# Optimization experiments

Measured on AMD Instinct MI355X. Metric: run time of the kernel, lower is better.

The kernel has to match this reference:

```python
import jax, jax.numpy as jnp
import numpy as np

B, N, E, F, C = 4, 10000, 160000, 128, 128
NUM_ITERATIONS = 3  # num_iterations init arg


def setup_inputs() -> dict:
    key = jax.random.key(0)
    ks = jax.random.split(key, 8)
    objects = jax.random.normal(ks[0], (B, N, F), dtype=jnp.float32)
    connections = jax.random.randint(ks[1], (B, E, 2), 0, N, dtype=jnp.int32)
    # small init scales keep exp() in the attention numerically tame (mirrors
    # glorot/orthogonal-scale weights at init)
    object_state_W = jax.random.normal(ks[2], (F, C), dtype=jnp.float32) * (1.0 / np.sqrt(F))
    state_attention_W = jax.random.normal(ks[3], (C, C), dtype=jnp.float32) * 0.05
    linked_state_attention_W = jax.random.normal(ks[4], (C, C), dtype=jnp.float32) * 0.05
    linked_state_W = jax.random.normal(ks[5], (C, C), dtype=jnp.float32) * (1.0 / np.sqrt(C))
    attention_b = jnp.zeros((C,), dtype=jnp.float32)
    state_b = jnp.zeros((C,), dtype=jnp.float32)
    return {
        "objects": objects,
        "object_state_W": object_state_W,
        "state_attention_W": state_attention_W,
        "linked_state_attention_W": linked_state_attention_W,
        "attention_b": attention_b,
        "linked_state_W": linked_state_W,
        "state_b": state_b,
        "connections": connections,
    }


def reference(objects, object_state_W, state_attention_W, linked_state_attention_W,
              attention_b, linked_state_W, state_b, connections):
    # bidirectional: double edges with both orientations  [B, 2E]
    src = jnp.concatenate([connections[:, :, 0], connections[:, :, 1]], axis=1)
    dst = jnp.concatenate([connections[:, :, 1], connections[:, :, 0]], axis=1)

    # initial states: [B, N, C]
    states = jnp.tanh(jnp.einsum('bnf,fc->bnc', objects, object_state_W) + state_b)

    def step_one(states_b, src_b, dst_b):
        # states_b: [N, C]; src_b/dst_b: [2E]
        states_aW = states_b @ state_attention_W          # [N, C]
        linked_aW = states_b @ linked_state_attention_W   # [N, C]
        # per-edge unnormalized attention  [2E, C]
        attention = jnp.exp(states_aW[src_b] + linked_aW[dst_b] + attention_b)
        # scatter-add normalization; self edge contributes 1 (exp(0))
        attention_norm = jnp.ones_like(states_b).at[src_b].add(attention)  # [N, C]
        self_attention = 1.0 / attention_norm
        attention = attention / attention_norm[src_b]
        # weighted neighbor aggregation
        attented = attention * states_b[dst_b]                              # [2E, C]
        linked_gated = jnp.zeros_like(states_b).at[src_b].add(attented)     # [N, C]
        return jnp.tanh(states_b * self_attention + linked_gated @ linked_state_W + state_b)

    step = jax.vmap(step_one)
    for _ in range(NUM_ITERATIONS):
        states = step(states, src, dst)
    return states
```

## Files before the change

### kernel.cpp

```cpp
#include <hip/hip_runtime.h>
#include <hip/hip_bf16.h>


#define BATCH 4
#define NNODE 10000
#define NEDGE 160000
#define TWOE  (2*NEDGE)
#define MROWS (BATCH*NNODE)
#define NCHUNK 64
#define CHUNKE (NEDGE/NCHUNK)
#define PADN  10240

typedef unsigned short u16;
typedef unsigned int   u32;
typedef __attribute__((ext_vector_type(8))) short bf16x8_t;
typedef __attribute__((ext_vector_type(4))) float f32x4_t;

__device__ __forceinline__ float b2f(u16 h){ return __uint_as_float(((u32)h) << 16); }
__device__ __forceinline__ u16 f2bf(float f){
  u32 u = __float_as_uint(f);
  return (u16)((u + 0x7fffu + ((u >> 16) & 1u)) >> 16);
}
__device__ __forceinline__ float fast_tanh(float x){
  float e = __expf(2.0f * x);
  return fmaf(-2.0f, __builtin_amdgcn_rcpf(e + 1.0f), 1.0f);
}

__global__ void detect_dtype(const u32* __restrict__ objw, int* __restrict__ flag){
  __shared__ int zc, hc;
  if (threadIdx.x == 0){ zc = 0; hc = 0; }
  __syncthreads();
  int z = 0, h = 0;
  for (int i = threadIdx.x; i < 1024; i += 256){
    u32 lo = objw[i] & 0xffffu;
    if (lo == 0) z++;
    if (((lo >> 7) & 0xffu) >= 160u) h++;
  }
  atomicAdd(&zc, z); atomicAdd(&hc, h);
  __syncthreads();
  if (threadIdx.x == 0) *flag = (hc > 0 || zc > 512) ? 1 : 0;
}

__global__ void prep_weights(const void* __restrict__ Wo, const void* __restrict__ Wa,
                             const void* __restrict__ Wla, const void* __restrict__ Wl,
                             const void* __restrict__ ab, const void* __restrict__ sb,
                             const int* __restrict__ flag, u16* __restrict__ Wt,
                             float* __restrict__ biasf){
  int idx = blockIdx.x * 256 + threadIdx.x;
  bool f = (*flag != 0);
  if (idx < 65536){
    int m = idx >> 14, k = (idx >> 7) & 127, c = idx & 127;
    const void* src = (m == 0) ? Wo : (m == 1) ? Wa : (m == 2) ? Wla : Wl;
    u16 h = f ? f2bf(((const float*)src)[k * 128 + c]) : ((const u16*)src)[k * 128 + c];
    Wt[m * 16384 + c * 128 + k] = h;
  } else {
    int t = idx - 65536;
    const void* src = (t < 128) ? sb : ab;
    int i = t & 127;
    biasf[t] = f ? ((const float*)src)[i] : b2f(((const u16*)src)[i]);
  }
}

__device__ __forceinline__ void chunk_of(int blk, int& b, int& c){
  int xcd = blk & 7;
  b = xcd >> 1;
  c = ((blk >> 3) << 1) | (xcd & 1);
}

__global__ void __launch_bounds__(256) csr_hist(const int* __restrict__ conn,
                                                u16* __restrict__ partial){
  int b, c; chunk_of(blockIdx.x, b, c);
  __shared__ u32 hist[NNODE];
  for (int n = threadIdx.x; n < NNODE; n += 256) hist[n] = 0;
  __syncthreads();
  const int2* cp = (const int2*)conn + (size_t)b * NEDGE + c * CHUNKE;
  for (int i = threadIdx.x; i < CHUNKE; i += 256){
    int2 e = cp[i];
    atomicAdd(&hist[e.x], 1);
    atomicAdd(&hist[e.y], 1);
  }
  __syncthreads();
  u16* prow = partial + (size_t)(b * NCHUNK + c) * PADN;
  for (int n = threadIdx.x; n < NNODE; n += 256) prow[n] = (u16)hist[n];
}

__global__ void __launch_bounds__(256) csr_colscan(u16* __restrict__ partial,
    int* __restrict__ row_start, int* __restrict__ bsum){
  int b = blockIdx.x / 40, w = blockIdx.x % 40;
  int n = w * 256 + threadIdx.x;
  u32 run = 0;
  if (n < NNODE){
    #pragma unroll 8
    for (int c = 0; c < NCHUNK; c++){
      size_t idx = (size_t)(b * NCHUNK + c) * PADN + n;
      u32 v = partial[idx];
      partial[idx] = (u16)run;
      run += v;
    }
  }
  __shared__ u32 buf[256];
  buf[threadIdx.x] = run;
  __syncthreads();
  for (int off = 1; off < 256; off <<= 1){
    u32 x = (threadIdx.x >= (unsigned)off) ? buf[threadIdx.x - off] : 0;
    __syncthreads();
    buf[threadIdx.x] += x;
    __syncthreads();
  }
  u32 incl = buf[threadIdx.x];
  if (n < NNODE) row_start[b * (NNODE + 1) + n] = (int)(incl - run);
  if (threadIdx.x == 255) bsum[blockIdx.x] = (int)incl;
}

__global__ void scanB(const int* __restrict__ bsum, int* __restrict__ boff,
                      int* __restrict__ row_start){
  __shared__ int s[160];
  if (threadIdx.x < 160) s[threadIdx.x] = bsum[threadIdx.x];
  __syncthreads();
  if (threadIdx.x < 160){
    int b = threadIdx.x / 40, j = threadIdx.x % 40;
    int off = 0;
    for (int q = b * 40; q < b * 40 + j; q++) off += s[q];
    boff[threadIdx.x] = off;
  }
  if (threadIdx.x < BATCH) row_start[threadIdx.x * (NNODE + 1) + NNODE] = TWOE;
}

__global__ void scanC(int* __restrict__ row_start, const int* __restrict__ boff){
  int b = blockIdx.x / 40, j = blockIdx.x % 40;
  int n = j * 256 + threadIdx.x;
  if (n < NNODE) row_start[b * (NNODE + 1) + n] += boff[blockIdx.x];
}

__global__ void __launch_bounds__(256) csr_fill(const int* __restrict__ conn,
    const u16* __restrict__ partial, const int* __restrict__ row_start,
    int* __restrict__ edge_dst){
  int b, c; chunk_of(blockIdx.x, b, c);
  __shared__ u32 cur[NNODE];
  const u16* prow = partial + (size_t)(b * NCHUNK + c) * PADN;
  const int* rs = row_start + b * (NNODE + 1);
  for (int n = threadIdx.x; n < NNODE; n += 256) cur[n] = (u32)rs[n] + prow[n];
  __syncthreads();
  const int2* cp = (const int2*)conn + (size_t)b * NEDGE + c * CHUNKE;
  int* edb = edge_dst + (size_t)b * TWOE;
  for (int i = threadIdx.x; i < CHUNKE; i += 256){
    int2 e = cp[i];
    u32 p1 = atomicAdd(&cur[e.x], 1); edb[p1] = e.y;
    u32 p2 = atomicAdd(&cur[e.y], 1); edb[p2] = e.x;
  }
}

__device__ __forceinline__ void gemm_tile4(const u16* __restrict__ arow,
    const u16* __restrict__ wt, int lm, int lq, int cofs, f32x4_t acc[4]){
  #pragma unroll
  for (int ks = 0; ks < 4; ks++){
    bf16x8_t a = *(const bf16x8_t*)(arow + ks * 32);
    #pragma unroll
    for (int nb = 0; nb < 4; nb++){
      bf16x8_t bfr = *(const bf16x8_t*)(wt + (cofs + nb * 16 + lm) * 128 + ks * 32 + lq * 8);
      acc[nb] = __builtin_amdgcn_mfma_f32_16x16x32_bf16(a, bfr, acc[nb], 0, 0, 0);
    }
  }
}

__device__ __forceinline__ void gemm_tile4_packed(const u32* __restrict__ Lrow,
    const u16* __restrict__ wt, int lm, int lq, int cofs, f32x4_t acc[4]){
  #pragma unroll
  for (int ks = 0; ks < 4; ks++){
    uint4 wa = *(const uint4*)(Lrow + ks * 32 + lq * 8);
    uint4 wb = *(const uint4*)(Lrow + ks * 32 + lq * 8 + 4);
    bf16x8_t a;
    a[0] = (short)wa.x; a[1] = (short)wa.y; a[2] = (short)wa.z; a[3] = (short)wa.w;
    a[4] = (short)wb.x; a[5] = (short)wb.y; a[6] = (short)wb.z; a[7] = (short)wb.w;
    #pragma unroll
    for (int nb = 0; nb < 4; nb++){
      bf16x8_t bfr = *(const bf16x8_t*)(wt + (cofs + nb * 16 + lm) * 128 + ks * 32 + lq * 8);
      acc[nb] = __builtin_amdgcn_mfma_f32_16x16x32_bf16(a, bfr, acc[nb], 0, 0, 0);
    }
  }
}

__device__ __forceinline__ void phase2_awlaw4(const u16* __restrict__ ldstile,
    const u16* __restrict__ Wt, const float* __restrict__ biasf,
    int lm, int lq, int cofs, int r0, _Float16* __restrict__ eat,
    u32* __restrict__ ghw){
  const u16* Wta  = Wt + 16384;
  const u16* Wtla = Wt + 32768;
  const u16* ldsrow = ldstile + lm * 136 + lq * 8;
  f32x4_t accA[4], accL[4];
  #pragma unroll
  for (int i = 0; i < 4; i++){ accA[i] = (f32x4_t){0.f,0.f,0.f,0.f}; accL[i] = (f32x4_t){0.f,0.f,0.f,0.f}; }
  #pragma unroll
  for (int ks = 0; ks < 4; ks++){
    bf16x8_t a = *(const bf16x8_t*)(ldsrow + ks * 32);
    #pragma unroll
    for (int nb = 0; nb < 4; nb++){
      bf16x8_t ba = *(const bf16x8_t*)(Wta  + (cofs + nb * 16 + lm) * 128 + ks * 32 + lq * 8);
      bf16x8_t bl = *(const bf16x8_t*)(Wtla + (cofs + nb * 16 + lm) * 128 + ks * 32 + lq * 8);
      accA[nb] = __builtin_amdgcn_mfma_f32_16x16x32_bf16(a, ba, accA[nb], 0, 0, 0);
      accL[nb] = __builtin_amdgcn_mfma_f32_16x16x32_bf16(a, bl, accL[nb], 0, 0, 0);
    }
  }
  #pragma unroll
  for (int nb = 0; nb < 4; nb++){
    int col = cofs + nb * 16 + lm;
    float bb = biasf[128 + col];
    #pragma unroll
    for (int i = 0; i < 4; i++){
      int row = r0 + lq * 4 + i;
      float ea = fminf(__expf(accA[nb][i]), 60000.0f);
      eat[(lq * 4 + i) * 128 + col] = (_Float16)ea;
      _Float16 elh = (_Float16)fminf(__expf(accL[nb][i] + bb), 60000.0f);
      u16 sbf = ldstile[(lq * 4 + i) * 136 + col];
      _Float16 sh = (_Float16)b2f(sbf);
      u32 elu = (u32)(*(const u16*)&elh);
      u32 shu = (u32)(*(const u16*)&sh);
      ghw[(size_t)row * 64 + (col & 63)] = elu | (shu << 16);
    }
  }
}

__device__ __forceinline__ void eah_writeback(const _Float16* __restrict__ eat,
    _Float16* __restrict__ eah, int blk_r0, int tid){
  const uint4* src = (const uint4*)eat;
  uint4* dst = (uint4*)(eah + (size_t)blk_r0 * 128);
  dst[tid]       = src[tid];
  dst[tid + 256] = src[tid + 256];
}

__global__ void __launch_bounds__(256) fused_init(const void* __restrict__ obj_raw,
    const int* __restrict__ flag, const u16* __restrict__ Wt,
    const float* __restrict__ biasf, _Float16* __restrict__ eah,
    u32* __restrict__ gat0, u32* __restrict__ gat1){
  __shared__ u16 lds[2][16 * 136];
  __shared__ _Float16 eat[2][16 * 128];
  const int lane = threadIdx.x & 63, wave = threadIdx.x >> 6;
  const int t = wave >> 1, ch = wave & 1, cofs = ch * 64;
  const int r0 = blockIdx.x * 32 + t * 16;
  const int lm = lane & 15, lq = lane >> 4;
  f32x4_t acc[4];
  #pragma unroll
  for (int i = 0; i < 4; i++) acc[i] = (f32x4_t){0.f, 0.f, 0.f, 0.f};
  if (*flag){
    const float* arow = (const float*)obj_raw + (size_t)(r0 + lm) * 128 + lq * 8;
    #pragma unroll
    for (int ks = 0; ks < 4; ks++){
      float4 fa = *(const float4*)(arow + ks * 32);
      float4 fb = *(const float4*)(arow + ks * 32 + 4);
      bf16x8_t a;
      a[0] = (short)f2bf(fa.x); a[1] = (short)f2bf(fa.y);
      a[2] = (short)f2bf(fa.z); a[3] = (short)f2bf(fa.w);
      a[4] = (short)f2bf(fb.x); a[5] = (short)f2bf(fb.y);
      a[6] = (short)f2bf(fb.z); a[7] = (short)f2bf(fb.w);
      #pragma unroll
      for (int nb = 0; nb < 4; nb++){
        bf16x8_t bfr = *(const bf16x8_t*)(Wt + (cofs + nb * 16 + lm) * 128 + ks * 32 + lq * 8);
        acc[nb] = __builtin_amdgcn_mfma_f32_16x16x32_bf16(a, bfr, acc[nb], 0, 0, 0);
      }
    }
  } else {
    gemm_tile4((const u16*)obj_raw + (size_t)(r0 + lm) * 128 + lq * 8, Wt, lm, lq, cofs, acc);
  }
  #pragma unroll
  for (int nb = 0; nb < 4; nb++){
    int col = cofs + nb * 16 + lm;
    float bb = biasf[col];
    #pragma unroll
    for (int i = 0; i < 4; i++)
      lds[t][(lq * 4 + i) * 136 + col] = f2bf(fast_tanh(acc[nb][i] + bb));
  }
  __syncthreads();
  phase2_awlaw4(&lds[t][0], Wt, biasf, lm, lq, cofs, r0, &eat[t][0], ch ? gat1 : gat0);
  __syncthreads();
  eah_writeback(&eat[0][0], eah, blockIdx.x * 32, threadIdx.x);
}

__global__ void __launch_bounds__(256) fused_mid(const u32* __restrict__ lgsa,
    const u16* __restrict__ Wt, const float* __restrict__ biasf,
    _Float16* __restrict__ eah, u32* __restrict__ gat0, u32* __restrict__ gat1){
  __shared__ u16 lds[2][16 * 136];
  __shared__ _Float16 eat[2][16 * 128];
  const int lane = threadIdx.x & 63, wave = threadIdx.x >> 6;
  const int t = wave >> 1, ch = wave & 1, cofs = ch * 64;
  const int r0 = blockIdx.x * 32 + t * 16;
  const int lm = lane & 15, lq = lane >> 4;
  f32x4_t acc[4];
  #pragma unroll
  for (int i = 0; i < 4; i++) acc[i] = (f32x4_t){0.f, 0.f, 0.f, 0.f};
  gemm_tile4_packed(lgsa + (size_t)(r0 + lm) * 128, Wt + 49152, lm, lq, cofs, acc);
  #pragma unroll
  for (int nb = 0; nb < 4; nb++){
    int col = cofs + nb * 16 + lm;
    float bb = biasf[col];
    #pragma unroll
    for (int i = 0; i < 4; i++){
      int row = r0 + lq * 4 + i;
      u32 v = lgsa[(size_t)row * 128 + col];
      u16 hb = (u16)(v >> 16);
      float sa = (float)(*(const _Float16*)&hb);
      lds[t][(lq * 4 + i) * 136 + col] = f2bf(fast_tanh(sa + acc[nb][i] + bb));
    }
  }
  __syncthreads();
  phase2_awlaw4(&lds[t][0], Wt, biasf, lm, lq, cofs, r0, &eat[t][0], ch ? gat1 : gat0);
  __syncthreads();
  eah_writeback(&eat[0][0], eah, blockIdx.x * 32, threadIdx.x);
}

__global__ void __launch_bounds__(256) final_out(const u32* __restrict__ lgsa,
    const u16* __restrict__ Wt, const float* __restrict__ biasf,
    const int* __restrict__ flag, void* __restrict__ outp){
  const int lane = threadIdx.x & 63, wave = threadIdx.x >> 6;
  const int t = wave >> 1, ch = wave & 1, cofs = ch * 64;
  const int r0 = blockIdx.x * 32 + t * 16;
  const int lm = lane & 15, lq = lane >> 4;
  bool f32out = (*flag != 0);
  f32x4_t acc[4];
  #pragma unroll
  for (int i = 0; i < 4; i++) acc[i] = (f32x4_t){0.f, 0.f, 0.f, 0.f};
  gemm_tile4_packed(lgsa + (size_t)(r0 + lm) * 128, Wt + 49152, lm, lq, cofs, acc);
  #pragma unroll
  for (int nb = 0; nb < 4; nb++){
    int col = cofs + nb * 16 + lm;
    float bb = biasf[col];
    #pragma unroll
    for (int i = 0; i < 4; i++){
      int row = r0 + lq * 4 + i;
      u32 vv = lgsa[(size_t)row * 128 + col];
      u16 hb = (u16)(vv >> 16);
      float sa = (float)(*(const _Float16*)&hb);
      float v = fast_tanh(sa + acc[nb][i] + bb);
      if (f32out) ((float*)outp)[(size_t)row * 128 + col] = v;
      else        ((u16*)  outp)[(size_t)row * 128 + col] = f2bf(v);
    }
  }
}

__device__ __forceinline__ void acc_mix(u32 g, float one, float& a1, float& a2){
  asm("v_fma_mix_f32 %0, %2, %3, %0 op_sel:[0,0,0] op_sel_hi:[1,0,0]\n\t"
      "v_fma_mix_f32 %1, %2, %2, %1 op_sel:[0,1,0] op_sel_hi:[1,1,0]"
      : "+v"(a1), "+v"(a2)
      : "v"(g), "v"(one));
}

__global__ void __launch_bounds__(256) edge_kernel(const _Float16* __restrict__ eah,
    const u32* __restrict__ gat0, const u32* __restrict__ gat1,
    const int* __restrict__ row_start, const int* __restrict__ edge_dst,
    u32* __restrict__ lgsa){
  int blk = blockIdx.x;
  int xcd = blk & 7;
  int b = xcd >> 1, h = xcd & 1;
  int i = blk >> 3;
  int n = i * 4 + (int)(threadIdx.x >> 6);
  int node = b * NNODE + n;
  int c = threadIdx.x & 63;
  const u32* gh = (h ? gat1 : gat0) + (size_t)b * NNODE * 64;
  const u32* ghc = gh + c;
  int e0 = __builtin_amdgcn_readfirstlane(row_start[b * (NNODE + 1) + n]);
  int e1 = __builtin_amdgcn_readfirstlane(row_start[b * (NNODE + 1) + n + 1]);
  const int* ed = edge_dst + (size_t)b * TWOE;

  float ea = (float)eah[(size_t)node * 128 + h * 64 + c];
  u32 self = ghc[(size_t)n << 6];
  const float one = 1.0f;

  float s1 = 0.f, s2 = 0.f, t1 = 0.f, t2 = 0.f;
  int len = e1 - e0;
  int e = e0;
  int rem = len >> 3;
  int d[8];
  if (rem){
    #pragma unroll
    for (int j = 0; j < 8; j++) d[j] = ed[e0 + j];
  }
  for (; rem > 0; rem--){
    u32 g[8];
    #pragma unroll
    for (int j = 0; j < 8; j++) g[j] = ghc[(size_t)d[j] << 6];
    int ep = e + (rem > 1 ? 8 : 0);
    int dn[8];
    #pragma unroll
    for (int j = 0; j < 8; j++) dn[j] = ed[ep + j];
    #pragma unroll
    for (int j = 0; j < 8; j++) acc_mix(g[j], one, (j & 1) ? t1 : s1, (j & 1) ? t2 : s2);
    #pragma unroll
    for (int j = 0; j < 8; j++) d[j] = dn[j];
    e += 8;
  }
  for (; e < e1; e++){
    u32 gg = ghc[(size_t)ed[e] << 6];
    acc_mix(gg, one, s1, s2);
  }
  s1 += t1; s2 += t2;
  float inv = __builtin_amdgcn_rcpf(fmaf(ea, s1, 1.0f));
  float lg = ea * s2 * inv;
  u16 hb = (u16)(self >> 16);
  float s_self = (float)(*(const _Float16*)&hb);
  _Float16 hs = (_Float16)(s_self * inv);
  u32 pk = (u32)f2bf(lg) | ((u32)(*(const u16*)&hs) << 16);
  lgsa[(size_t)node * 128 + h * 64 + c] = pk;
}

extern "C" void kernel_launch(void* const* d_in, const int* in_sizes, int n_in,
                              void* d_out, int out_size, void* d_ws, size_t ws_size,
                              hipStream_t stream){
  (void)in_sizes; (void)n_in; (void)ws_size; (void)out_size;
  const void* objects = d_in[0];
  const void* Wo      = d_in[1];
  const void* Wa      = d_in[2];
  const void* Wla     = d_in[3];
  const void* attn_b  = d_in[4];
  const void* Wl      = d_in[5];
  const void* state_b = d_in[6];
  const int*  conn    = (const int*)d_in[7];

  char* base = (char*)d_ws;
  size_t off = 0;
  auto alloc = [&](size_t bytes) -> char* {
    char* p = base + off;
    off = (off + bytes + 255) & ~(size_t)255;
    return p;
  };
  int*      flag      = (int*)     alloc(256);
  u16*      Wt        = (u16*)     alloc((size_t)4 * 16384 * 2);
  float*    biasf     = (float*)   alloc(256 * 4);
  _Float16* eah       = (_Float16*)alloc((size_t)MROWS * 128 * 2);
  u32*      gat0      = (u32*)     alloc((size_t)MROWS * 64 * 4);
  u32*      gat1      = (u32*)     alloc((size_t)MROWS * 64 * 4);
  u32*      lgsa      = (u32*)     alloc((size_t)MROWS * 128 * 4);
  u16*      partial   = (u16*)     alloc((size_t)BATCH * NCHUNK * PADN * 2);
  int*      row_start = (int*)     alloc((size_t)BATCH * (NNODE + 1) * 4);
  int*      edge_dst  = (int*)     alloc((size_t)BATCH * TWOE * 4);
  int*      bsum      = (int*)     alloc(160 * 4);
  int*      boff      = (int*)     alloc(160 * 4);

  detect_dtype<<<1, 256, 0, stream>>>((const u32*)objects, flag);
  prep_weights<<<257, 256, 0, stream>>>(Wo, Wa, Wla, Wl, attn_b, state_b, flag, Wt, biasf);

  csr_hist<<<256, 256, 0, stream>>>(conn, partial);
  csr_colscan<<<160, 256, 0, stream>>>(partial, row_start, bsum);
  scanB<<<1, 256, 0, stream>>>(bsum, boff, row_start);
  scanC<<<160, 256, 0, stream>>>(row_start, boff);
  csr_fill<<<256, 256, 0, stream>>>(conn, partial, row_start, edge_dst);

  fused_init<<<MROWS / 32, 256, 0, stream>>>(objects, flag, Wt, biasf, eah, gat0, gat1);
  edge_kernel<<<MROWS / 2, 256, 0, stream>>>(eah, gat0, gat1, row_start, edge_dst, lgsa);
  fused_mid<<<MROWS / 32, 256, 0, stream>>>(lgsa, Wt, biasf, eah, gat0, gat1);
  edge_kernel<<<MROWS / 2, 256, 0, stream>>>(eah, gat0, gat1, row_start, edge_dst, lgsa);
  fused_mid<<<MROWS / 32, 256, 0, stream>>>(lgsa, Wt, biasf, eah, gat0, gat1);
  edge_kernel<<<MROWS / 2, 256, 0, stream>>>(eah, gat0, gat1, row_start, edge_dst, lgsa);
  final_out<<<MROWS / 32, 256, 0, stream>>>(lgsa, Wt, biasf, flag, d_out);
}
```

Baseline: 375.6 us.

## Pad CSR rows to multiples of eight with zero sentinel nodes for tail-free gather

Each node's adjacency list is padded to a multiple of 8 entries, and the padding points at per-batch sentinel rows whose gathered values are zeroed, so the edge kernel no longer needs a scalar tail loop. The edge kernel reads indices with readfirstlane as scalars, double-buffers two groups of 8 gathers ahead of the accumulation, and sets an occupancy launch bound. This costs two extra setup kernels, a degree buffer and a larger edge array. The main risk is that the sentinel indexing across batches must land exactly on the zeroed rows.

```diff
diff --git a/kernel.cpp b/kernel.cpp
--- a/kernel.cpp
+++ b/kernel.cpp
@@ -10,6 +10,7 @@
 #define NCHUNK 64
 #define CHUNKE (NEDGE/NCHUNK)
 #define PADN  10240
+#define EDPAD (TWOE + 8*NNODE)
 
 typedef unsigned short u16;
 typedef unsigned int   u32;
@@ -85,7 +86,7 @@
 }
 
 __global__ void __launch_bounds__(256) csr_colscan(u16* __restrict__ partial,
-    int* __restrict__ row_start, int* __restrict__ bsum){
+    int* __restrict__ row_start, int* __restrict__ bsum, int* __restrict__ deg){
   int b = blockIdx.x / 40, w = blockIdx.x % 40;
   int n = w * 256 + threadIdx.x;
   u32 run = 0;
@@ -98,8 +99,9 @@
       run += v;
     }
   }
+  u32 pad = (run + 7u) & ~7u;
   __shared__ u32 buf[256];
-  buf[threadIdx.x] = run;
+  buf[threadIdx.x] = pad;
   __syncthreads();
   for (int off = 1; off < 256; off <<= 1){
     u32 x = (threadIdx.x >= (unsigned)off) ? buf[threadIdx.x - off] : 0;
@@ -108,7 +110,10 @@
     __syncthreads();
   }
   u32 incl = buf[threadIdx.x];
-  if (n < NNODE) row_start[b * (NNODE + 1) + n] = (int)(incl - run);
+  if (n < NNODE){
+    row_start[b * (NNODE + 1) + n] = (int)(incl - pad);
+    deg[b * NNODE + n] = (int)run;
+  }
   if (threadIdx.x == 255) bsum[blockIdx.x] = (int)incl;
 }
 
@@ -123,7 +128,11 @@
     for (int q = b * 40; q < b * 40 + j; q++) off += s[q];
     boff[threadIdx.x] = off;
   }
-  if (threadIdx.x < BATCH) row_start[threadIdx.x * (NNODE + 1) + NNODE] = TWOE;
+  if (threadIdx.x < BATCH){
+    int tot = 0;
+    for (int q = threadIdx.x * 40; q < threadIdx.x * 40 + 40; q++) tot += s[q];
+    row_start[threadIdx.x * (NNODE + 1) + NNODE] = tot;
+  }
 }
 
 __global__ void scanC(int* __restrict__ row_start, const int* __restrict__ boff){
@@ -142,12 +151,31 @@
   for (int n = threadIdx.x; n < NNODE; n += 256) cur[n] = (u32)rs[n] + prow[n];
   __syncthreads();
   const int2* cp = (const int2*)conn + (size_t)b * NEDGE + c * CHUNKE;
-  int* edb = edge_dst + (size_t)b * TWOE;
+  int* edb = edge_dst + (size_t)b * EDPAD;
   for (int i = threadIdx.x; i < CHUNKE; i += 256){
     int2 e = cp[i];
     u32 p1 = atomicAdd(&cur[e.x], 1); edb[p1] = e.y;
     u32 p2 = atomicAdd(&cur[e.y], 1); edb[p2] = e.x;
   }
+}
+
+__global__ void pad_fill(const int* __restrict__ row_start,
+                         const int* __restrict__ deg, int* __restrict__ edge_dst){
+  int b = blockIdx.x / 40, j = blockIdx.x % 40;
+  int n = j * 256 + threadIdx.x;
+  if (n >= NNODE) return;
+  const int* rs = row_start + b * (NNODE + 1);
+  int s = rs[n] + deg[b * NNODE + n];
+  int epad = rs[n + 1];
+  int sent = 40000 - 9999 * b;
+  int* edb = edge_dst + (size_t)b * EDPAD;
+  for (int p = s; p < epad; p++) edb[p] = sent;
+}
+
+__global__ void zero_sent(u32* __restrict__ g0, u32* __restrict__ g1){
+  size_t base = (size_t)MROWS * 64;
+  g0[base + threadIdx.x] = 0;
+  g1[base + threadIdx.x] = 0;
 }
 
 __device__ __forceinline__ void gemm_tile4(const u16* __restrict__ arow,
@@ -343,7 +371,12 @@
       : "v"(g), "v"(one));
 }
 
-__global__ void __launch_bounds__(256) edge_kernel(const _Float16* __restrict__ eah,
+__device__ __forceinline__ u32 gath1(const u32* __restrict__ gh, int d, int c){
+  const u32* p = (const u32*)((const char*)gh + ((size_t)(u32)d << 8));
+  return p[c];
+}
+
+__global__ void __launch_bounds__(256, 8) edge_kernel(const _Float16* __restrict__ eah,
     const u32* __restrict__ gat0, const u32* __restrict__ gat1,
     const int* __restrict__ row_start, const int* __restrict__ edge_dst,
     u32* __restrict__ lgsa){
@@ -355,42 +388,61 @@
   int node = b * NNODE + n;
   int c = threadIdx.x & 63;
   const u32* gh = (h ? gat1 : gat0) + (size_t)b * NNODE * 64;
-  const u32* ghc = gh + c;
   int e0 = __builtin_amdgcn_readfirstlane(row_start[b * (NNODE + 1) + n]);
   int e1 = __builtin_amdgcn_readfirstlane(row_start[b * (NNODE + 1) + n + 1]);
-  const int* ed = edge_dst + (size_t)b * TWOE;
+  const int* ed = edge_dst + (size_t)b * EDPAD;
 
   float ea = (float)eah[(size_t)node * 128 + h * 64 + c];
-  u32 self = ghc[(size_t)n << 6];
+  u32 self = gh[((size_t)n << 6) + c];
   const float one = 1.0f;
 
   float s1 = 0.f, s2 = 0.f, t1 = 0.f, t2 = 0.f;
-  int len = e1 - e0;
-  int e = e0;
-  int rem = len >> 3;
-  int d[8];
-  if (rem){
-    #pragma unroll
-    for (int j = 0; j < 8; j++) d[j] = ed[e0 + j];
-  }
-  for (; rem > 0; rem--){
-    u32 g[8];
-    #pragma unroll
-    for (int j = 0; j < 8; j++) g[j] = ghc[(size_t)d[j] << 6];
-    int ep = e + (rem > 1 ? 8 : 0);
-    int dn[8];
-    #pragma unroll
-    for (int j = 0; j < 8; j++) dn[j] = ed[ep + j];
-    #pragma unroll
-    for (int j = 0; j < 8; j++) acc_mix(g[j], one, (j & 1) ? t1 : s1, (j & 1) ? t2 : s2);
-    #pragma unroll
-    for (int j = 0; j < 8; j++) d[j] = dn[j];
+  int ng = (e1 - e0) >> 3;
+  if (ng){
+    int dB[8]; u32 g[8], gn[8];
+    int e = e0;
+    { const int* ep = ed + e;
+      #pragma unroll
+      for (int j = 0; j < 8; j++) dB[j] = __builtin_amdgcn_readfirstlane(ep[j]); }
+    #pragma unroll
+    for (int j = 0; j < 8; j++) g[j] = gath1(gh, dB[j], c);
     e += 8;
-  }
-  for (; e < e1; e++){
-    u32 gg = ghc[(size_t)ed[e] << 6];
-    acc_mix(gg, one, s1, s2);
-  }
+    { const int* ep = ed + e;
+      #pragma unroll
+      for (int j = 0; j < 8; j++) dB[j] = __builtin_amdgcn_readfirstlane(ep[j]); }
+    e += 8;
+    int k = 1;
+    for (; k + 1 < ng; k += 2){
+      #pragma unroll
+      for (int j = 0; j < 8; j++) gn[j] = gath1(gh, dB[j], c);
+      { const int* ep = ed + e;
+        #pragma unroll
+        for (int j = 0; j < 8; j++) dB[j] = __builtin_amdgcn_readfirstlane(ep[j]); }
+      e += 8;
+      #pragma unroll
+      for (int j = 0; j < 8; j++) acc_mix(g[j], one, (j & 1) ? t1 : s1, (j & 1) ? t2 : s2);
+      #pragma unroll
+      for (int j = 0; j < 8; j++) g[j] = gath1(gh, dB[j], c);
+      { const int* ep = ed + e;
+        #pragma unroll
+        for (int j = 0; j < 8; j++) dB[j] = __builtin_amdgcn_readfirstlane(ep[j]); }
+      e += 8;
+      #pragma unroll
+      for (int j = 0; j < 8; j++) acc_mix(gn[j], one, (j & 1) ? t1 : s1, (j & 1) ? t2 : s2);
+    }
+    if (k < ng){
+      #pragma unroll
+      for (int j = 0; j < 8; j++) gn[j] = gath1(gh, dB[j], c);
+      #pragma unroll
+      for (int j = 0; j < 8; j++) acc_mix(g[j], one, (j & 1) ? t1 : s1, (j & 1) ? t2 : s2);
+      #pragma unroll
+      for (int j = 0; j < 8; j++) acc_mix(gn[j], one, (j & 1) ? t1 : s1, (j & 1) ? t2 : s2);
+    } else {
+      #pragma unroll
+      for (int j = 0; j < 8; j++) acc_mix(g[j], one, (j & 1) ? t1 : s1, (j & 1) ? t2 : s2);
+    }
+  }
+
   s1 += t1; s2 += t2;
   float inv = __builtin_amdgcn_rcpf(fmaf(ea, s1, 1.0f));
   float lg = ea * s2 * inv;
@@ -425,12 +477,13 @@
   u16*      Wt        = (u16*)     alloc((size_t)4 * 16384 * 2);
   float*    biasf     = (float*)   alloc(256 * 4);
   _Float16* eah       = (_Float16*)alloc((size_t)MROWS * 128 * 2);
-  u32*      gat0      = (u32*)     alloc((size_t)MROWS * 64 * 4);
-  u32*      gat1      = (u32*)     alloc((size_t)MROWS * 64 * 4);
+  u32*      gat0      = (u32*)     alloc((size_t)(MROWS + 4) * 64 * 4);
+  u32*      gat1      = (u32*)     alloc((size_t)(MROWS + 4) * 64 * 4);
   u32*      lgsa      = (u32*)     alloc((size_t)MROWS * 128 * 4);
   u16*      partial   = (u16*)     alloc((size_t)BATCH * NCHUNK * PADN * 2);
   int*      row_start = (int*)     alloc((size_t)BATCH * (NNODE + 1) * 4);
-  int*      edge_dst  = (int*)     alloc((size_t)BATCH * TWOE * 4);
+  int*      edge_dst  = (int*)     alloc((size_t)BATCH * EDPAD * 4);
+  int*      deg       = (int*)     alloc((size_t)MROWS * 4);
   int*      bsum      = (int*)     alloc(160 * 4);
   int*      boff      = (int*)     alloc(160 * 4);
 
@@ -438,10 +491,12 @@
   prep_weights<<<257, 256, 0, stream>>>(Wo, Wa, Wla, Wl, attn_b, state_b, flag, Wt, biasf);
 
   csr_hist<<<256, 256, 0, stream>>>(conn, partial);
-  csr_colscan<<<160, 256, 0, stream>>>(partial, row_start, bsum);
+  csr_colscan<<<160, 256, 0, stream>>>(partial, row_start, bsum, deg);
   scanB<<<1, 256, 0, stream>>>(bsum, boff, row_start);
   scanC<<<160, 256, 0, stream>>>(row_start, boff);
   csr_fill<<<256, 256, 0, stream>>>(conn, partial, row_start, edge_dst);
+  pad_fill<<<160, 256, 0, stream>>>(row_start, deg, edge_dst);
+  zero_sent<<<1, 256, 0, stream>>>(gat0, gat1);
 
   fused_init<<<MROWS / 32, 256, 0, stream>>>(objects, flag, Wt, biasf, eah, gat0, gat1);
   edge_kernel<<<MROWS / 2, 256, 0, stream>>>(eah, gat0, gat1, row_start, edge_dst, lgsa);
```

Measured after the change: 359.1 us. 1.05x faster.
